# Optimization experiments

Measured on AMD Instinct MI355X. Metric: run time of the kernel, lower is better.

The kernel has to match this reference:

```python
import jax, jax.numpy as jnp
import numpy as np
import math

R = 3  # search_radius (init_kwargs)


def _normalize(x, eps=1e-6):
    # F.normalize(x, dim=1): x / max(||x||_2, eps)
    n = jnp.sqrt(jnp.sum(x * x, axis=1, keepdims=True))
    return x / jnp.maximum(n, eps)


def setup_inputs() -> dict:
    key = jax.random.key(0)
    k1, k2 = jax.random.split(key)
    B, D, H, W = 8, 64, 256, 256
    rubin_2d = jax.random.normal(k1, (B, D, H, W), dtype=jnp.float32)
    vis_2d = jax.random.normal(k2, (B, D, H, W), dtype=jnp.float32)
    log_temperature = jnp.asarray(math.log(0.1), dtype=jnp.float32)
    return {"rubin_2d": rubin_2d, "vis_2d": vis_2d, "log_temperature": log_temperature}


def reference(rubin_2d, vis_2d, log_temperature):
    B, D, H, W = rubin_2d.shape
    r = R
    K = (2 * r + 1) ** 2
    rubin_n = _normalize(rubin_2d)
    vis_n = _normalize(vis_2d)
    # replicate padding == 'edge'
    vis_pad = jnp.pad(vis_n, ((0, 0), (0, 0), (r, r), (r, r)), mode="edge")
    scale = 1.0 / math.sqrt(float(max(1, D)))
    # K=(2r+1)^2 shifted correlation maps (small fixed loop over displacements)
    corrs = []
    for dy in range(-r, r + 1):
        for dx in range(-r, r + 1):
            shifted = vis_pad[:, :, r + dy:r + dy + H, r + dx:r + dx + W]
            corrs.append(jnp.sum(rubin_n * shifted, axis=1) * scale)  # [B,H,W]
    logits = jnp.stack(corrs, axis=1)  # [B,K,H,W]

    offs = np.arange(-r, r + 1, dtype=np.float32)
    dy_lut = jnp.asarray(np.repeat(offs, 2 * r + 1)).reshape(1, K, 1, 1)
    dx_lut = jnp.asarray(np.tile(offs, 2 * r + 1)).reshape(1, K, 1, 1)

    tau = jnp.maximum(jnp.exp(log_temperature), 1e-3)
    probs_local = jax.nn.softmax(logits / tau, axis=1)  # [B,K,H,W]
    dy_local = jnp.sum(probs_local * dy_lut, axis=1, keepdims=True)
    dx_local = jnp.sum(probs_local * dx_lut, axis=1, keepdims=True)
    conf_local = jnp.max(probs_local, axis=1, keepdims=True)

    logits_global = jnp.mean(logits, axis=(2, 3), keepdims=True)  # [B,K,1,1]
    probs_global = jax.nn.softmax(logits_global / tau, axis=1)
    dy_global = jnp.sum(probs_global * dy_lut, axis=1, keepdims=True)
    dx_global = jnp.sum(probs_global * dx_lut, axis=1, keepdims=True)
    conf_global = jnp.max(probs_global, axis=1, keepdims=True)

    uniform = 1.0 / float(max(1, K))
    local_weight = jnp.clip((conf_local - uniform) / max(1e-6, 1.0 - uniform), 0.0, 1.0)
    dy = local_weight * dy_local + (1.0 - local_weight) * dy_global
    dx = local_weight * dx_local + (1.0 - local_weight) * dx_global
    return (dy, dx, conf_local, conf_global, local_weight, logits)
```

## Files before the change

kernel.cpp:

```cpp
#include <hip/hip_runtime.h>

#define HDIM 256
#define WDIM 256
#define DDIM 64
#define HWSZ (HDIM*WDIM)
#define NPIX 524288

#define TW 32
#define TH 16
#define BT 512
#define HW_T 38
#define HH_T 22
#define NPX 836
#define DC 8
#define NCH 8
#define PSTR 12

#define OFF_DY   0
#define OFF_DX   524288
#define OFF_CONF 1048576
#define OFF_CG   1572864
#define OFF_LW   1572872
#define OFF_LG   2097160

#define WS_GACC 0
#define WS_DYG  392
#define WS_DXG  400

__global__ void zero_ws_k(float* __restrict__ ws) {
    const int i = threadIdx.x;
    if (i < 408) ws[i] = 0.f;
}

__global__ void __launch_bounds__(BT, 4)
corr_main_k(const float* __restrict__ rub, const float* __restrict__ vis,
            const float* __restrict__ ltemp, float* __restrict__ out,
            float* __restrict__ ws)
{
    __shared__ __align__(16) float vis_s[NPX * PSTR];
    __shared__ float invv_s[NPX];
    __shared__ float gacc_s[49];

    const int tid = threadIdx.x;
    const int tx  = tid & 31;
    const int ty  = tid >> 5;
    const int w0  = blockIdx.x * TW;
    const int h0  = blockIdx.y * TH;
    const int b   = blockIdx.z;
    const int ibase = b * (DDIM * HWSZ);

    if (tid < 49) gacc_s[tid] = 0.f;

    const bool val1 = (tid + BT) < NPX;
    const int px1c  = val1 ? (tid + BT) : (NPX - 1);
    auto halo_goff = [&](int px) -> int {
        const int hr = px / HW_T;
        const int wc = px - hr * HW_T;
        const int gh = min(HDIM - 1, max(0, h0 - 3 + hr));
        const int gw = min(WDIM - 1, max(0, w0 - 3 + wc));
        return gh * WDIM + gw;
    };
    const int goff0 = halo_goff(tid);
    const int goff1 = halo_goff(px1c);
    const int pown  = (h0 + ty) * WDIM + (w0 + tx);
    const int l0 = tid * PSTR;
    const int l1 = px1c * PSTR;

    float acc[49];
#pragma unroll
    for (int k = 0; k < 49; ++k) acc[k] = 0.f;
    float sq0 = 0.f, sq1 = 0.f, sr = 0.f;

    float vv0[DC], vv1[DC], rcur[DC], rnext[DC];
#pragma unroll
    for (int d = 0; d < DC; ++d) {
        const int gof = ibase + d * HWSZ;
        vv0[d]  = vis[gof + goff0];
        vv1[d]  = vis[gof + goff1];
        rcur[d] = rub[gof + pown];
    }

    const float* vb = &vis_s[(ty * HW_T + tx) * PSTR];

#pragma unroll 1
    for (int c = 0; c < NCH; ++c) {
        __syncthreads();
        *reinterpret_cast<float4*>(&vis_s[l0])     = make_float4(vv0[0], vv0[1], vv0[2], vv0[3]);
        *reinterpret_cast<float4*>(&vis_s[l0 + 4]) = make_float4(vv0[4], vv0[5], vv0[6], vv0[7]);
        *reinterpret_cast<float4*>(&vis_s[l1])     = make_float4(vv1[0], vv1[1], vv1[2], vv1[3]);
        *reinterpret_cast<float4*>(&vis_s[l1 + 4]) = make_float4(vv1[4], vv1[5], vv1[6], vv1[7]);
#pragma unroll
        for (int d = 0; d < DC; ++d) { sq0 += vv0[d] * vv0[d]; sq1 += vv1[d] * vv1[d]; }
        __syncthreads();

        if (c < NCH - 1) {
#pragma unroll
            for (int d = 0; d < DC; ++d) {
                const int gof = ibase + ((c + 1) * DC + d) * HWSZ;
                vv0[d]  = vis[gof + goff0];
                vv1[d]  = vis[gof + goff1];
                rnext[d] = rub[gof + pown];
            }
        }

#pragma unroll
        for (int g = 0; g < 2; ++g) {
            const float a0 = rcur[4*g+0], a1 = rcur[4*g+1], a2 = rcur[4*g+2], a3 = rcur[4*g+3];
#pragma unroll
            for (int dyi = 0; dyi < 7; ++dyi) {
#pragma unroll
                for (int dxi = 0; dxi < 7; ++dxi) {
                    const float4 v = *reinterpret_cast<const float4*>(
                        vb + (dyi * HW_T + dxi) * PSTR + 4 * g);
                    float a = acc[dyi * 7 + dxi];
                    a = fmaf(a0, v.x, a); a = fmaf(a1, v.y, a);
                    a = fmaf(a2, v.z, a); a = fmaf(a3, v.w, a);
                    acc[dyi * 7 + dxi] = a;
                }
            }
        }
#pragma unroll
        for (int d = 0; d < DC; ++d) sr += rcur[d] * rcur[d];
#pragma unroll
        for (int d = 0; d < DC; ++d) rcur[d] = rnext[d];
    }

    invv_s[tid] = 1.f / fmaxf(sqrtf(sq0), 1e-6f);
    if (val1) invv_s[tid + BT] = 1.f / fmaxf(sqrtf(sq1), 1e-6f);
    __syncthreads();

    const float tau  = fmaxf(__expf(ltemp[0]), 1e-3f);
    const float itau = 1.f / tau;
    const float invr = 1.f / fmaxf(sqrtf(sr), 1e-6f);
    const float cR   = invr * 0.125f;
    const float uu   = 1.f / 49.f;
    const float i1mu = 49.f / 48.f;

    const int h = h0 + ty, w = w0 + tx;
    const int lgbase = OFF_LG + b * 49 * HWSZ + h * WDIM + w;
    float mlg = -1e30f;
#pragma unroll
    for (int dyi = 0; dyi < 7; ++dyi) {
        const int rowb = (ty + dyi) * HW_T + tx;
#pragma unroll
        for (int dxi = 0; dxi < 7; ++dxi) {
            const int k = dyi * 7 + dxi;
            const float lg = acc[k] * cR * invv_s[rowb + dxi];
            out[lgbase + k * HWSZ] = lg;
            acc[k] = lg;
            mlg = fmaxf(mlg, lg);
        }
    }
    const float m = mlg * itau;
    float S = 0.f, sdy = 0.f, sdx = 0.f;
#pragma unroll
    for (int dyi = 0; dyi < 7; ++dyi) {
#pragma unroll
        for (int dxi = 0; dxi < 7; ++dxi) {
            const float e = __expf(fmaf(acc[dyi * 7 + dxi], itau, -m));
            S += e;
            sdy += e * (float)(dyi - 3);
            sdx += e * (float)(dxi - 3);
        }
    }
    const float invS = 1.f / S;
    const float conf = invS;
    const float lw   = fminf(fmaxf((conf - uu) * i1mu, 0.f), 1.f);
    const int po = b * HWSZ + h * WDIM + w;
    out[OFF_CONF + po] = conf;
    out[OFF_LW   + po] = lw;
    out[OFF_DY   + po] = sdy * invS;
    out[OFF_DX   + po] = sdx * invS;

#pragma unroll
    for (int k = 0; k < 49; ++k) {
        float v = acc[k];
#pragma unroll
        for (int off = 32; off > 0; off >>= 1)
            v += __shfl_xor(v, off, 64);
        if ((tid & 63) == 0) atomicAdd(&gacc_s[k], v);
    }
    __syncthreads();
    if (tid < 49) atomicAdd(&ws[WS_GACC + b * 49 + tid], gacc_s[tid]);
}

__global__ void glob_branch_k(const float* __restrict__ ltemp,
                              float* __restrict__ out, float* __restrict__ ws)
{
    const int t = threadIdx.x;
    if (t >= 8) return;
    const float tau  = fmaxf(__expf(ltemp[0]), 1e-3f);
    const float itau = 1.f / tau;
    float tk[49];
    float m = -1e30f;
#pragma unroll
    for (int k = 0; k < 49; ++k) {
        const float mean = ws[WS_GACC + t * 49 + k] * (1.f / 65536.f);
        tk[k] = mean * itau;
        m = fmaxf(m, tk[k]);
    }
    float S = 0.f, sdy = 0.f, sdx = 0.f;
#pragma unroll
    for (int k = 0; k < 49; ++k) {
        const float e = __expf(tk[k] - m);
        S += e;
        sdy += e * (float)(k / 7 - 3);
        sdx += e * (float)(k % 7 - 3);
    }
    const float invS = 1.f / S;
    out[OFF_CG + t] = invS;
    ws[WS_DYG + t] = sdy * invS;
    ws[WS_DXG + t] = sdx * invS;
}

__global__ void combine_k(float* __restrict__ out, const float* __restrict__ ws)
{
    const int gid = blockIdx.x * 256 + threadIdx.x;
    if (gid >= NPIX) return;
    const int b = gid >> 16;
    const float lw  = out[OFF_LW + gid];
    const float dyl = out[OFF_DY + gid];
    const float dxl = out[OFF_DX + gid];
    out[OFF_DY + gid] = lw * dyl + (1.f - lw) * ws[WS_DYG + b];
    out[OFF_DX + gid] = lw * dxl + (1.f - lw) * ws[WS_DXG + b];
}

extern "C" void kernel_launch(void* const* d_in, const int* in_sizes, int n_in,
                              void* d_out, int out_size, void* d_ws, size_t ws_size,
                              hipStream_t stream)
{
    const float* rub = (const float*)d_in[0];
    const float* vis = (const float*)d_in[1];
    const float* lt  = (const float*)d_in[2];
    float* out = (float*)d_out;
    float* ws  = (float*)d_ws;

    hipLaunchKernelGGL(zero_ws_k, dim3(1), dim3(512), 0, stream, ws);
    hipLaunchKernelGGL(corr_main_k, dim3(WDIM / TW, HDIM / TH, 8), dim3(BT), 0, stream,
                       rub, vis, lt, out, ws);
    hipLaunchKernelGGL(glob_branch_k, dim3(1), dim3(64), 0, stream, lt, out, ws);
    hipLaunchKernelGGL(combine_k, dim3(NPIX / 256), dim3(256), 0, stream, out, ws);
}
```

Measured before the change: 394.0 us.

## Pack vis tile to fp16 in LDS and use fdot2 for correlation

The shared-memory vis halo tile now stores 8 channels as packed fp16 pairs (16 bytes per pixel instead of 48), and rubin values are converted to f16x2 in registers. The inner 49-displacement loop uses v_dot2 (fp16 inputs with fp32 accumulation) in place of scalar fp32 FMAs, cutting LDS traffic and ALU instructions by about half. This lowers the precision of the logits, which could break tolerance against the fp32 reference. Norms are still computed in fp32.

```diff
diff --git a/kernel.cpp b/kernel.cpp
--- a/kernel.cpp
+++ b/kernel.cpp
@@ -14,7 +14,32 @@
 #define NPX 836
 #define DC 8
 #define NCH 8
-#define PSTR 12
+
+typedef _Float16 f16;
+typedef __attribute__((ext_vector_type(2))) _Float16 f16x2;
+
+#if defined(__has_builtin)
+# if __has_builtin(__builtin_amdgcn_fdot2)
+#  define HAVE_FDOT2 1
+# endif
+#endif
+
+__device__ __forceinline__ float fdot2(f16x2 a, f16x2 b, float c) {
+#ifdef HAVE_FDOT2
+    return __builtin_amdgcn_fdot2(a, b, c, false);
+#else
+    return c + (float)a.x * (float)b.x + (float)a.y * (float)b.y;
+#endif
+}
+
+__device__ __forceinline__ float pk2(float a, float b) {
+    f16x2 t; t.x = (f16)a; t.y = (f16)b;
+    return __builtin_bit_cast(float, t);
+}
+
+__device__ __forceinline__ f16x2 bc(float x) {
+    return __builtin_bit_cast(f16x2, x);
+}
 
 #define OFF_DY   0
 #define OFF_DX   524288
@@ -37,7 +62,7 @@
             const float* __restrict__ ltemp, float* __restrict__ out,
             float* __restrict__ ws)
 {
-    __shared__ __align__(16) float vis_s[NPX * PSTR];
+    __shared__ __align__(16) float vis_s[NPX * 4];
     __shared__ float invv_s[NPX];
     __shared__ float gacc_s[49];
 
@@ -63,66 +88,67 @@
     const int goff0 = halo_goff(tid);
     const int goff1 = halo_goff(px1c);
     const int pown  = (h0 + ty) * WDIM + (w0 + tx);
-    const int l0 = tid * PSTR;
-    const int l1 = px1c * PSTR;
+    const int l0 = tid * 4;
+    const int l1 = px1c * 4;
 
     float acc[49];
 #pragma unroll
     for (int k = 0; k < 49; ++k) acc[k] = 0.f;
     float sq0 = 0.f, sq1 = 0.f, sr = 0.f;
 
-    float vv0[DC], vv1[DC], rcur[DC], rnext[DC];
+    float vv0[DC], vv1[DC], rn[DC];
 #pragma unroll
     for (int d = 0; d < DC; ++d) {
         const int gof = ibase + d * HWSZ;
-        vv0[d]  = vis[gof + goff0];
-        vv1[d]  = vis[gof + goff1];
-        rcur[d] = rub[gof + pown];
-    }
-
-    const float* vb = &vis_s[(ty * HW_T + tx) * PSTR];
+        vv0[d] = vis[gof + goff0];
+        vv1[d] = vis[gof + goff1];
+        rn[d]  = rub[gof + pown];
+    }
+
+    const float* vb = vis_s + (ty * HW_T + tx) * 4;
+    f16x2 rh[4];
 
 #pragma unroll 1
     for (int c = 0; c < NCH; ++c) {
         __syncthreads();
-        *reinterpret_cast<float4*>(&vis_s[l0])     = make_float4(vv0[0], vv0[1], vv0[2], vv0[3]);
-        *reinterpret_cast<float4*>(&vis_s[l0 + 4]) = make_float4(vv0[4], vv0[5], vv0[6], vv0[7]);
-        *reinterpret_cast<float4*>(&vis_s[l1])     = make_float4(vv1[0], vv1[1], vv1[2], vv1[3]);
-        *reinterpret_cast<float4*>(&vis_s[l1 + 4]) = make_float4(vv1[4], vv1[5], vv1[6], vv1[7]);
+        *reinterpret_cast<float4*>(&vis_s[l0]) =
+            make_float4(pk2(vv0[0], vv0[1]), pk2(vv0[2], vv0[3]),
+                        pk2(vv0[4], vv0[5]), pk2(vv0[6], vv0[7]));
+        *reinterpret_cast<float4*>(&vis_s[l1]) =
+            make_float4(pk2(vv1[0], vv1[1]), pk2(vv1[2], vv1[3]),
+                        pk2(vv1[4], vv1[5]), pk2(vv1[6], vv1[7]));
 #pragma unroll
         for (int d = 0; d < DC; ++d) { sq0 += vv0[d] * vv0[d]; sq1 += vv1[d] * vv1[d]; }
+#pragma unroll
+        for (int j = 0; j < 4; ++j) { f16x2 t; t.x = (f16)rn[2*j]; t.y = (f16)rn[2*j+1]; rh[j] = t; }
+#pragma unroll
+        for (int d = 0; d < DC; ++d) sr += rn[d] * rn[d];
         __syncthreads();
 
         if (c < NCH - 1) {
 #pragma unroll
             for (int d = 0; d < DC; ++d) {
                 const int gof = ibase + ((c + 1) * DC + d) * HWSZ;
-                vv0[d]  = vis[gof + goff0];
-                vv1[d]  = vis[gof + goff1];
-                rnext[d] = rub[gof + pown];
+                vv0[d] = vis[gof + goff0];
+                vv1[d] = vis[gof + goff1];
+                rn[d]  = rub[gof + pown];
             }
         }
 
 #pragma unroll
-        for (int g = 0; g < 2; ++g) {
-            const float a0 = rcur[4*g+0], a1 = rcur[4*g+1], a2 = rcur[4*g+2], a3 = rcur[4*g+3];
-#pragma unroll
-            for (int dyi = 0; dyi < 7; ++dyi) {
-#pragma unroll
-                for (int dxi = 0; dxi < 7; ++dxi) {
-                    const float4 v = *reinterpret_cast<const float4*>(
-                        vb + (dyi * HW_T + dxi) * PSTR + 4 * g);
-                    float a = acc[dyi * 7 + dxi];
-                    a = fmaf(a0, v.x, a); a = fmaf(a1, v.y, a);
-                    a = fmaf(a2, v.z, a); a = fmaf(a3, v.w, a);
-                    acc[dyi * 7 + dxi] = a;
-                }
+        for (int dyi = 0; dyi < 7; ++dyi) {
+#pragma unroll
+            for (int dxi = 0; dxi < 7; ++dxi) {
+                const float4 v = *reinterpret_cast<const float4*>(
+                    vb + (dyi * HW_T + dxi) * 4);
+                float a = acc[dyi * 7 + dxi];
+                a = fdot2(rh[0], bc(v.x), a);
+                a = fdot2(rh[1], bc(v.y), a);
+                a = fdot2(rh[2], bc(v.z), a);
+                a = fdot2(rh[3], bc(v.w), a);
+                acc[dyi * 7 + dxi] = a;
             }
         }
-#pragma unroll
-        for (int d = 0; d < DC; ++d) sr += rcur[d] * rcur[d];
-#pragma unroll
-        for (int d = 0; d < DC; ++d) rcur[d] = rnext[d];
     }
 
     invv_s[tid] = 1.f / fmaxf(sqrtf(sq0), 1e-6f);
```

Measured after the change: 386.9 us. No clear change (-1.8%).

## Compute shifted correlations with fp16 MFMA over full-depth LDS halo tile

Applied to the files above, without the earlier changes.

Replaces the scalar FMA correlation loop with 16x16x32 fp16 MFMA instructions. The whole 64-channel halo tile of vis is staged once into LDS as packed halves, and each wave computes 16-pixel by 16-column correlation blocks, then scatters the diagonal band through a per-wave LDS scratch buffer to gather the 49 logits. Softmax and global accumulation are split across lane groups with shuffle reductions. This trades fp32 accuracy for fp16 inputs and lowers occupancy (launch bounds 2) because of the larger LDS footprint and register arrays.

```diff
diff --git a/kernel.cpp b/kernel.cpp
--- a/kernel.cpp
+++ b/kernel.cpp
@@ -9,12 +9,10 @@
 #define TW 32
 #define TH 16
 #define BT 512
-#define HW_T 38
-#define HH_T 22
-#define NPX 836
-#define DC 8
-#define NCH 8
-#define PSTR 12
+#define HR 22
+#define HC 38
+#define NHP 836
+#define PXF4 9
 
 #define OFF_DY   0
 #define OFF_DX   524288
@@ -27,158 +25,187 @@
 #define WS_DYG  392
 #define WS_DXG  400
 
+typedef _Float16 f16;
+typedef __attribute__((ext_vector_type(8))) _Float16 f16x8;
+typedef __attribute__((ext_vector_type(4))) float f32x4;
+
+__device__ __forceinline__ float pk2(float a, float b) {
+    union { f16 h[2]; float f; } u;
+    u.h[0] = (f16)a; u.h[1] = (f16)b;
+    return u.f;
+}
+
 __global__ void zero_ws_k(float* __restrict__ ws) {
     const int i = threadIdx.x;
     if (i < 408) ws[i] = 0.f;
 }
 
-__global__ void __launch_bounds__(BT, 4)
+__global__ void __launch_bounds__(BT, 2)
 corr_main_k(const float* __restrict__ rub, const float* __restrict__ vis,
             const float* __restrict__ ltemp, float* __restrict__ out,
             float* __restrict__ ws)
 {
-    __shared__ __align__(16) float vis_s[NPX * PSTR];
-    __shared__ float invv_s[NPX];
+    __shared__ __align__(16) float vis_s[NHP * 36];
+    __shared__ float invv_s[NHP];
+    __shared__ float tb[8 * 16 * 52];
     __shared__ float gacc_s[49];
 
-    const int tid = threadIdx.x;
-    const int tx  = tid & 31;
-    const int ty  = tid >> 5;
-    const int w0  = blockIdx.x * TW;
-    const int h0  = blockIdx.y * TH;
-    const int b   = blockIdx.z;
+    const int tid  = threadIdx.x;
+    const int wv   = tid >> 6;
+    const int lane = tid & 63;
+    const int g    = lane >> 4;
+    const int n    = lane & 15;
+    const int w0 = blockIdx.x * TW;
+    const int h0 = blockIdx.y * TH;
+    const int b  = blockIdx.z;
     const int ibase = b * (DDIM * HWSZ);
 
     if (tid < 49) gacc_s[tid] = 0.f;
 
-    const bool val1 = (tid + BT) < NPX;
-    const int px1c  = val1 ? (tid + BT) : (NPX - 1);
-    auto halo_goff = [&](int px) -> int {
-        const int hr = px / HW_T;
-        const int wc = px - hr * HW_T;
-        const int gh = min(HDIM - 1, max(0, h0 - 3 + hr));
-        const int gw = min(WDIM - 1, max(0, w0 - 3 + wc));
-        return gh * WDIM + gw;
-    };
-    const int goff0 = halo_goff(tid);
-    const int goff1 = halo_goff(px1c);
-    const int pown  = (h0 + ty) * WDIM + (w0 + tx);
-    const int l0 = tid * PSTR;
-    const int l1 = px1c * PSTR;
-
-    float acc[49];
-#pragma unroll
-    for (int k = 0; k < 49; ++k) acc[k] = 0.f;
-    float sq0 = 0.f, sq1 = 0.f, sr = 0.f;
-
-    float vv0[DC], vv1[DC], rcur[DC], rnext[DC];
-#pragma unroll
-    for (int d = 0; d < DC; ++d) {
-        const int gof = ibase + d * HWSZ;
-        vv0[d]  = vis[gof + goff0];
-        vv1[d]  = vis[gof + goff1];
-        rcur[d] = rub[gof + pown];
-    }
-
-    const float* vb = &vis_s[(ty * HW_T + tx) * PSTR];
-
-#pragma unroll 1
-    for (int c = 0; c < NCH; ++c) {
-        __syncthreads();
-        *reinterpret_cast<float4*>(&vis_s[l0])     = make_float4(vv0[0], vv0[1], vv0[2], vv0[3]);
-        *reinterpret_cast<float4*>(&vis_s[l0 + 4]) = make_float4(vv0[4], vv0[5], vv0[6], vv0[7]);
-        *reinterpret_cast<float4*>(&vis_s[l1])     = make_float4(vv1[0], vv1[1], vv1[2], vv1[3]);
-        *reinterpret_cast<float4*>(&vis_s[l1 + 4]) = make_float4(vv1[4], vv1[5], vv1[6], vv1[7]);
-#pragma unroll
-        for (int d = 0; d < DC; ++d) { sq0 += vv0[d] * vv0[d]; sq1 += vv1[d] * vv1[d]; }
-        __syncthreads();
-
-        if (c < NCH - 1) {
-#pragma unroll
-            for (int d = 0; d < DC; ++d) {
-                const int gof = ibase + ((c + 1) * DC + d) * HWSZ;
-                vv0[d]  = vis[gof + goff0];
-                vv1[d]  = vis[gof + goff1];
-                rnext[d] = rub[gof + pown];
-            }
-        }
-
-#pragma unroll
-        for (int g = 0; g < 2; ++g) {
-            const float a0 = rcur[4*g+0], a1 = rcur[4*g+1], a2 = rcur[4*g+2], a3 = rcur[4*g+3];
-#pragma unroll
-            for (int dyi = 0; dyi < 7; ++dyi) {
-#pragma unroll
-                for (int dxi = 0; dxi < 7; ++dxi) {
-                    const float4 v = *reinterpret_cast<const float4*>(
-                        vb + (dyi * HW_T + dxi) * PSTR + 4 * g);
-                    float a = acc[dyi * 7 + dxi];
-                    a = fmaf(a0, v.x, a); a = fmaf(a1, v.y, a);
-                    a = fmaf(a2, v.z, a); a = fmaf(a3, v.w, a);
-                    acc[dyi * 7 + dxi] = a;
-                }
-            }
-        }
-#pragma unroll
-        for (int d = 0; d < DC; ++d) sr += rcur[d] * rcur[d];
-#pragma unroll
-        for (int d = 0; d < DC; ++d) rcur[d] = rnext[d];
-    }
-
-    invv_s[tid] = 1.f / fmaxf(sqrtf(sq0), 1e-6f);
-    if (val1) invv_s[tid + BT] = 1.f / fmaxf(sqrtf(sq1), 1e-6f);
+#pragma unroll
+    for (int rep = 0; rep < 2; ++rep) {
+        const int p = tid + rep * BT;
+        if (p < NHP) {
+            const int hr = p / HC, wc = p - hr * HC;
+            const int gof = min(HDIM-1, max(0, h0-3+hr)) * WDIM
+                          + min(WDIM-1, max(0, w0-3+wc));
+            float v[64];
+#pragma unroll
+            for (int d = 0; d < 64; ++d) v[d] = vis[ibase + d * HWSZ + gof];
+            float ssq = 0.f;
+#pragma unroll
+            for (int d = 0; d < 64; ++d) ssq = fmaf(v[d], v[d], ssq);
+#pragma unroll
+            for (int blk = 0; blk < 8; ++blk)
+                reinterpret_cast<float4*>(vis_s)[p * PXF4 + blk] =
+                    make_float4(pk2(v[blk*8+0], v[blk*8+1]), pk2(v[blk*8+2], v[blk*8+3]),
+                                pk2(v[blk*8+4], v[blk*8+5]), pk2(v[blk*8+6], v[blk*8+7]));
+            invv_s[p] = 1.f / fmaxf(sqrtf(ssq), 1e-6f);
+        }
+    }
+
+    const int sc   = wv >> 2;
+    const int wrow = wv & 3;
+    const int wgx  = w0 + sc * 16 + n;
+    float ar[4][16];
+#pragma unroll
+    for (int s = 0; s < 4; ++s) {
+        const int h = h0 + wrow * 4 + s;
+        const int base = ibase + h * WDIM + wgx + g * 8 * HWSZ;
+#pragma unroll
+        for (int j = 0; j < 8; ++j) {
+            ar[s][j]     = rub[base + j * HWSZ];
+            ar[s][8 + j] = rub[base + (32 + j) * HWSZ];
+        }
+    }
+
     __syncthreads();
 
     const float tau  = fmaxf(__expf(ltemp[0]), 1e-3f);
     const float itau = 1.f / tau;
-    const float invr = 1.f / fmaxf(sqrtf(sr), 1e-6f);
-    const float cR   = invr * 0.125f;
-    const float uu   = 1.f / 49.f;
-    const float i1mu = 49.f / 48.f;
-
-    const int h = h0 + ty, w = w0 + tx;
-    const int lgbase = OFF_LG + b * 49 * HWSZ + h * WDIM + w;
-    float mlg = -1e30f;
-#pragma unroll
-    for (int dyi = 0; dyi < 7; ++dyi) {
-        const int rowb = (ty + dyi) * HW_T + tx;
-#pragma unroll
-        for (int dxi = 0; dxi < 7; ++dxi) {
-            const int k = dyi * 7 + dxi;
-            const float lg = acc[k] * cR * invv_s[rowb + dxi];
-            out[lgbase + k * HWSZ] = lg;
-            acc[k] = lg;
-            mlg = fmaxf(mlg, lg);
-        }
-    }
-    const float m = mlg * itau;
-    float S = 0.f, sdy = 0.f, sdx = 0.f;
-#pragma unroll
-    for (int dyi = 0; dyi < 7; ++dyi) {
-#pragma unroll
-        for (int dxi = 0; dxi < 7; ++dxi) {
-            const float e = __expf(fmaf(acc[dyi * 7 + dxi], itau, -m));
-            S += e;
-            sdy += e * (float)(dyi - 3);
-            sdx += e * (float)(dxi - 3);
-        }
-    }
-    const float invS = 1.f / S;
-    const float conf = invS;
-    const float lw   = fminf(fmaxf((conf - uu) * i1mu, 0.f), 1.f);
-    const int po = b * HWSZ + h * WDIM + w;
-    out[OFF_CONF + po] = conf;
-    out[OFF_LW   + po] = lw;
-    out[OFF_DY   + po] = sdy * invS;
-    out[OFF_DX   + po] = sdx * invS;
-
-#pragma unroll
-    for (int k = 0; k < 49; ++k) {
-        float v = acc[k];
-#pragma unroll
-        for (int off = 32; off > 0; off >>= 1)
-            v += __shfl_xor(v, off, 64);
-        if ((tid & 63) == 0) atomicAdd(&gacc_s[k], v);
+    float tk[13];
+#pragma unroll
+    for (int m = 0; m < 13; ++m) tk[m] = 0.f;
+
+    const f16x8* vp = reinterpret_cast<const f16x8*>(vis_s);
+    float* tbw = &tb[wv * (16 * 52)];
+    const f32x4 zz = {0.f, 0.f, 0.f, 0.f};
+
+#pragma unroll 1
+    for (int s = 0; s < 4; ++s) {
+        const int ly = wrow * 4 + s;
+        const int h  = h0 + ly;
+
+        f16x8 ha0, ha1;
+#pragma unroll
+        for (int j = 0; j < 8; ++j) { ha0[j] = (f16)ar[s][j]; ha1[j] = (f16)ar[s][8+j]; }
+        float ssqa = 0.f;
+#pragma unroll
+        for (int j = 0; j < 16; ++j) ssqa = fmaf(ar[s][j], ar[s][j], ssqa);
+        ssqa += __shfl_xor(ssqa, 16, 64);
+        ssqa += __shfl_xor(ssqa, 32, 64);
+        const float sA = 0.125f / fmaxf(sqrtf(ssqa), 1e-6f);
+
+        const int kap = n - 4 * g;
+#pragma unroll
+        for (int dyi = 0; dyi < 7; ++dyi) {
+            const int row = ly + dyi;
+            const int c0  = sc * 16 + n;
+            const int c1  = min(37, sc * 16 + 16 + n);
+            const int p0  = (row * HC + c0) * PXF4;
+            const int p1  = (row * HC + c1) * PXF4;
+            f32x4 a0 = zz, a1 = zz;
+            a0 = __builtin_amdgcn_mfma_f32_16x16x32_f16(ha0, vp[p0 + g],     a0, 0, 0, 0);
+            a0 = __builtin_amdgcn_mfma_f32_16x16x32_f16(ha1, vp[p0 + 4 + g], a0, 0, 0, 0);
+            a1 = __builtin_amdgcn_mfma_f32_16x16x32_f16(ha0, vp[p1 + g],     a1, 0, 0, 0);
+            a1 = __builtin_amdgcn_mfma_f32_16x16x32_f16(ha1, vp[p1 + 4 + g], a1, 0, 0, 0);
+            const float iv0 = invv_s[row * HC + c0];
+            const float iv1 = invv_s[row * HC + c1];
+            const int kb = dyi * 7;
+#pragma unroll
+            for (int r = 0; r < 4; ++r) {
+                const int t0 = kap - r;
+                if ((unsigned)t0 <= 6u) tbw[(4*g + r) * 52 + kb + t0] = a0[r] * iv0;
+                const int t1 = kap - r + 16;
+                if ((unsigned)t1 <= 6u) tbw[(4*g + r) * 52 + kb + t1] = a1[r] * iv1;
+            }
+        }
+
+        float lgv[13];
+        float M = -1e30f;
+#pragma unroll
+        for (int m = 0; m < 13; ++m) {
+            const int k = g + 4 * m;
+            if (k < 49) {
+                const float lg = tbw[n * 52 + k] * sA;
+                lgv[m] = lg;
+                out[OFF_LG + b * (49 * HWSZ) + k * HWSZ + h * WDIM + w0 + sc*16 + n] = lg;
+                tk[m] += lg;
+                M = fmaxf(M, lg);
+            }
+        }
+        M = fmaxf(M, __shfl_xor(M, 16, 64));
+        M = fmaxf(M, __shfl_xor(M, 32, 64));
+        const float mm = M * itau;
+        float S = 0.f, sdy = 0.f, sdx = 0.f;
+#pragma unroll
+        for (int m = 0; m < 13; ++m) {
+            const int k = g + 4 * m;
+            if (k < 49) {
+                const float e = __expf(fmaf(lgv[m], itau, -mm));
+                const int dyk = (k * 37) >> 8;
+                const int dxk = k - dyk * 7;
+                S += e; sdy += e * (float)(dyk - 3); sdx += e * (float)(dxk - 3);
+            }
+        }
+        S   += __shfl_xor(S, 16, 64);   S   += __shfl_xor(S, 32, 64);
+        sdy += __shfl_xor(sdy, 16, 64); sdy += __shfl_xor(sdy, 32, 64);
+        sdx += __shfl_xor(sdx, 16, 64); sdx += __shfl_xor(sdx, 32, 64);
+        if (g == 0) {
+            const float invS = 1.f / S;
+            const float conf = invS;
+            const float lw = fminf(fmaxf((conf - 1.f/49.f) * (49.f/48.f), 0.f), 1.f);
+            const int po = b * HWSZ + h * WDIM + w0 + sc * 16 + n;
+            out[OFF_CONF + po] = conf;
+            out[OFF_LW   + po] = lw;
+            out[OFF_DY   + po] = sdy * invS;
+            out[OFF_DX   + po] = sdx * invS;
+        }
+    }
+
+#pragma unroll
+    for (int m = 0; m < 13; ++m) {
+        float v = tk[m];
+        v += __shfl_xor(v, 1, 64); v += __shfl_xor(v, 2, 64);
+        v += __shfl_xor(v, 4, 64); v += __shfl_xor(v, 8, 64);
+        tk[m] = v;
+    }
+    if (n == 0) {
+#pragma unroll
+        for (int m = 0; m < 13; ++m) {
+            const int k = g + 4 * m;
+            if (k < 49) atomicAdd(&gacc_s[k], tk[m]);
+        }
     }
     __syncthreads();
     if (tid < 49) atomicAdd(&ws[WS_GACC + b * 49 + tid], gacc_s[tid]);
@@ -191,18 +218,18 @@
     if (t >= 8) return;
     const float tau  = fmaxf(__expf(ltemp[0]), 1e-3f);
     const float itau = 1.f / tau;
-    float tk[49];
+    float tkk[49];
     float m = -1e30f;
 #pragma unroll
     for (int k = 0; k < 49; ++k) {
         const float mean = ws[WS_GACC + t * 49 + k] * (1.f / 65536.f);
-        tk[k] = mean * itau;
-        m = fmaxf(m, tk[k]);
+        tkk[k] = mean * itau;
+        m = fmaxf(m, tkk[k]);
     }
     float S = 0.f, sdy = 0.f, sdx = 0.f;
 #pragma unroll
     for (int k = 0; k < 49; ++k) {
-        const float e = __expf(tk[k] - m);
+        const float e = __expf(tkk[k] - m);
         S += e;
         sdy += e * (float)(k / 7 - 3);
         sdx += e * (float)(k % 7 - 3);
```

After: 430.0 us. 1.09x slower.
